# Performance work log

Hardware: AMD Instinct MI355X
Metric: run time of the kernel (lower is better)

## Reference

```python
import jax, jax.numpy as jnp
import numpy as np

B, N, NEV, E, D, L = 4, 20000, 100000, 400000, 64, 3

def setup_inputs() -> dict:
    key = jax.random.key(0)
    ks = jax.random.split(key, 12)
    x = jax.random.normal(ks[0], (B, N, 3), dtype=jnp.float32)
    # channel 0 is the susceptible boolean mask (0/1)
    mask0 = (jax.random.uniform(ks[1], (B, N)) < 0.3).astype(jnp.float32)
    x = x.at[..., 0].set(mask0)
    dag_edge_index = jax.random.randint(ks[2], (2, E), 0, NEV, dtype=jnp.int64)
    event_to_node = jax.random.randint(ks[3], (NEV,), 0, N, dtype=jnp.int64)
    event_src_node = jax.random.randint(ks[4], (NEV,), 0, N, dtype=jnp.int64)
    s = 1.0 / np.sqrt(D)
    Wp = jax.random.normal(ks[5], (6, D), dtype=jnp.float32) * (1.0 / np.sqrt(6))
    bp = jnp.zeros((D,), dtype=jnp.float32)
    Ws = jax.random.normal(ks[6], (L, D, D), dtype=jnp.float32) * s
    Wa = jax.random.normal(ks[7], (L, D, D), dtype=jnp.float32) * s
    ba = jnp.zeros((L, D), dtype=jnp.float32)
    Wo = jax.random.normal(ks[8], (D,), dtype=jnp.float32) * s
    bo = jnp.zeros((), dtype=jnp.float32)
    return {"x": x, "Wp": Wp, "bp": bp, "Ws": Ws, "Wa": Wa, "ba": ba,
            "Wo": Wo, "bo": bo, "dag_edge_index": dag_edge_index,
            "event_to_node": event_to_node, "event_src_node": event_src_node}

def reference(x, Wp, bp, Ws, Wa, ba, Wo, bo, dag_edge_index, event_to_node, event_src_node):
    n_events = event_src_node.shape[0]
    # event features: [B, n_events, 6] -> project -> ReLU
    ev_feat = jnp.concatenate([x[:, event_src_node, :], x[:, event_to_node, :]], axis=-1)
    h = jax.nn.relu(ev_feat @ Wp + bp)  # [B, n_events, D]
    # reversed DAG edges: src = dag[1], dst = dag[0]
    src_e, dst_e = dag_edge_index[1], dag_edge_index[0]
    deg = jnp.zeros((n_events,), h.dtype).at[dst_e].add(1.0)
    deg = jnp.maximum(deg, 1.0)[None, :, None]
    for l in range(Ws.shape[0]):
        agg = jnp.zeros_like(h).at[:, dst_e].add(h[:, src_e])  # scatter-add mean agg
        h = jax.nn.relu(h @ Ws[l] + (agg / deg) @ Wa[l] + ba[l])
    # aggregate events back to nodes (mean)
    node_emb = jnp.zeros((x.shape[0], x.shape[1], h.shape[-1]), h.dtype).at[:, event_to_node].add(h)
    count = jnp.zeros((x.shape[1],), h.dtype).at[event_to_node].add(1.0)
    node_emb = node_emb / jnp.maximum(count, 1.0)[None, :, None]
    scores = node_emb @ Wo + bo  # [B, N]
    susceptible = x[..., 0] > 0
    scores = jnp.where(susceptible, -jnp.inf, scores)
    return jax.nn.log_softmax(scores, axis=-1)
```

## Files before the change

kernel.cpp:

```cpp
#include <hip/hip_runtime.h>
#include <hip/hip_bf16.h>
#include <math.h>

constexpr int B   = 4;
constexpr int N   = 20000;
constexpr int NEV = 100000;
constexpr int E   = 400000;
constexpr int D   = 64;
constexpr int L   = 3;
constexpr int XS  = 136;
constexpr int CAP = 32;
constexpr int CHUNK = 625;

typedef short  short8 __attribute__((ext_vector_type(8)));
typedef float  f32x4  __attribute__((ext_vector_type(4)));
typedef float  f32x2  __attribute__((ext_vector_type(2)));


__device__ inline unsigned short f2bu(float f) {
  union { __hip_bfloat16 b; unsigned short s; } u;
  u.b = __float2bfloat16(f);
  return u.s;
}
__device__ inline unsigned packbf(float lo, float hi) {
  return ((unsigned)f2bu(hi) << 16) | (unsigned)f2bu(lo);
}


__global__ void k_zero(float4* __restrict__ p, int n4) {
  int i = blockIdx.x * blockDim.x + threadIdx.x;
  if (i < n4) p[i] = make_float4(0.f, 0.f, 0.f, 0.f);
}

__global__ void k_fill(const int* __restrict__ dag,
                       int* __restrict__ cnt,
                       int* __restrict__ csrc) {
  int i = blockIdx.x * blockDim.x + threadIdx.x;
  if (i >= E) return;
  int dst = dag[i];
  int src = dag[E + i];
  int pos = atomicAdd(&cnt[dst], 1);
  if (pos < CAP) csrc[dst * CAP + pos] = src;
}

__global__ void k_aux(const int* __restrict__ e2n,
                      int* __restrict__ ncount,
                      const float* __restrict__ Ws,
                      const float* __restrict__ Wa,
                      unsigned short* __restrict__ Wt) {
  int bid = blockIdx.x;
  if (bid < 391) {
    int i = bid * 256 + threadIdx.x;
    if (i < NEV) atomicAdd(&ncount[e2n[i]], 1);
  } else {
    int i = (bid - 391) * 256 + threadIdx.x;
    int l = i >> 13;
    int r = i & 8191;
    int n = r >> 7;
    int s = r & 127;
    int sl = (s < 64) ? s : s - 64;
    int c  = (sl & 3) * 16 + (sl >> 2);
    float v = (s < 64) ? Ws[l * 4096 + c * 64 + n]
                       : Wa[l * 4096 + c * 64 + n];
    Wt[l * 8192 + n * 128 + s] = f2bu(v);
  }
}

__global__ __launch_bounds__(256) void k_proj(const float* __restrict__ x,
                                              const float* __restrict__ Wp,
                                              const float* __restrict__ bp,
                                              const int* __restrict__ esrc,
                                              const int* __restrict__ e2n,
                                              unsigned* __restrict__ h) {
  int gid = blockIdx.x * blockDim.x + threadIdx.x;
  int p   = gid & 15;
  int row = gid >> 4;
  int e   = row >> 2;
  int b   = row & 3;
  int sn = esrc[e], tn = e2n[e];
  const float* xs = x + (size_t)(b * N + sn) * 3;
  const float* xt = x + (size_t)(b * N + tn) * 3;
  float xv[6] = {xs[0], xs[1], xs[2], xt[0], xt[1], xt[2]};
  float a[4];
#pragma unroll
  for (int t = 0; t < 4; ++t) {
    int d = p + 16 * t;
    float acc = bp[d];
#pragma unroll
    for (int k = 0; k < 6; ++k) acc += xv[k] * Wp[k * 64 + d];
    a[t] = fmaxf(acc, 0.f);
  }
  int w = __builtin_amdgcn_cvt_pk_fp8_f32(a[0], a[1], 0, false);
  w     = __builtin_amdgcn_cvt_pk_fp8_f32(a[2], a[3], w, true);
  h[row * 16 + p] = (unsigned)w;
}

template <bool LAST>
__global__ __launch_bounds__(256, 6) void k_layer(
    const unsigned short* __restrict__ Wt,
    const float* __restrict__ ba,
    const float* __restrict__ Wo,
    const int* __restrict__ e2n,
    const int* __restrict__ cnt,
    const int* __restrict__ csrc,
    const unsigned char* __restrict__ h_in,
    unsigned char* __restrict__ h_out,
    float* __restrict__ nscore) {
  __shared__ unsigned short sX[64 * XS];
  const int tid  = threadIdx.x;
  const int wv   = tid >> 6, lane = tid & 63;
  const int e0   = blockIdx.x * 16;
  const int r0   = e0 * 4;

  {
    uint4 v = *(const uint4*)(h_in + (size_t)r0 * 64 + tid * 16);
    int row = tid >> 2, ch = tid & 3;
    unsigned vv[4] = {v.x, v.y, v.z, v.w};
    unsigned out[8];
#pragma unroll
    for (int i = 0; i < 4; ++i) {
      f32x2 lo = __builtin_amdgcn_cvt_pk_f32_fp8((int)vv[i], false);
      f32x2 hi = __builtin_amdgcn_cvt_pk_f32_fp8((int)vv[i], true);
      out[2 * i]     = packbf(lo[0], lo[1]);
      out[2 * i + 1] = packbf(hi[0], hi[1]);
    }
    unsigned short* dst = sX + row * XS + ch * 16;
    *(uint4*)dst       = *(uint4*)&out[0];
    *(uint4*)(dst + 8) = *(uint4*)&out[4];
  }

  const int qg = lane >> 4, sub = lane & 15;
  int vidx = csrc[(size_t)(e0 + wv * 4 + qg) * CAP + sub];
  int c_l  = cnt[e0 + wv * 4 + (lane & 3)];

#pragma unroll
  for (int ei = 0; ei < 4; ++ei) {
    int c = __shfl(c_l, ei, 64);
    int cc16 = min(c, 16);
    float a[16];
#pragma unroll
    for (int i = 0; i < 16; ++i) a[i] = 0.f;
    for (int p = 0; p < cc16; p += 4) {
      int j = p + qg;
      if (j < cc16) {
        int s = __shfl(vidx, ei * 16 + j, 64);
        uint4 v = *(const uint4*)(h_in + (size_t)s * 256 + sub * 16);
        unsigned vv[4] = {v.x, v.y, v.z, v.w};
#pragma unroll
        for (int i = 0; i < 4; ++i) {
          f32x2 lo = __builtin_amdgcn_cvt_pk_f32_fp8((int)vv[i], false);
          f32x2 hi = __builtin_amdgcn_cvt_pk_f32_fp8((int)vv[i], true);
          a[4 * i + 0] += lo[0]; a[4 * i + 1] += lo[1];
          a[4 * i + 2] += hi[0]; a[4 * i + 3] += hi[1];
        }
      }
    }
    int cc = min(c, CAP);
    for (int j = 16 + qg; j < cc; j += 4) {
      int s = csrc[(size_t)(e0 + wv * 4 + ei) * CAP + j];
      uint4 v = *(const uint4*)(h_in + (size_t)s * 256 + sub * 16);
      unsigned vv[4] = {v.x, v.y, v.z, v.w};
#pragma unroll
      for (int i = 0; i < 4; ++i) {
        f32x2 lo = __builtin_amdgcn_cvt_pk_f32_fp8((int)vv[i], false);
        f32x2 hi = __builtin_amdgcn_cvt_pk_f32_fp8((int)vv[i], true);
        a[4 * i + 0] += lo[0]; a[4 * i + 1] += lo[1];
        a[4 * i + 2] += hi[0]; a[4 * i + 3] += hi[1];
      }
    }
#pragma unroll
    for (int i = 0; i < 16; ++i) {
      a[i] += __shfl_xor(a[i], 16, 64);
      a[i] += __shfl_xor(a[i], 32, 64);
    }
    if (qg == 0) {
      float inv = 1.f / fmaxf((float)c, 1.f);
      int lrow = (wv * 4 + ei) * 4 + (sub >> 2);
      unsigned out[8];
#pragma unroll
      for (int i = 0; i < 8; ++i)
        out[i] = packbf(a[2 * i] * inv, a[2 * i + 1] * inv);
      unsigned short* dst = sX + lrow * XS + 64 + (sub & 3) * 16;
      *(uint4*)dst       = *(uint4*)&out[0];
      *(uint4*)(dst + 8) = *(uint4*)&out[4];
    }
  }
  __syncthreads();

  const int m = lane & 15, q = lane >> 4;
  f32x4 acc[4];
#pragma unroll
  for (int t = 0; t < 4; ++t) {
    float bv = ba[t * 16 + m];
    acc[t] = (f32x4){bv, bv, bv, bv};
  }
  const unsigned short* xbase = sX + (wv * 16 + m) * XS + q * 8;
  const unsigned short* wbase = Wt + m * 128 + q * 8;
#pragma unroll
  for (int kk = 0; kk < 4; ++kk) {
    short8 av = *(const short8*)(xbase + kk * 32);
#pragma unroll
    for (int t = 0; t < 4; ++t) {
      short8 bv = *(const short8*)(wbase + t * 2048 + kk * 32);
      acc[t] = __builtin_amdgcn_mfma_f32_16x16x32_bf16(av, bv, acc[t], 0, 0, 0);
    }
  }

  if constexpr (!LAST) {
#pragma unroll
    for (int r = 0; r < 4; ++r) {
      int w = __builtin_amdgcn_cvt_pk_fp8_f32(fmaxf(acc[0][r], 0.f),
                                              fmaxf(acc[1][r], 0.f), 0, false);
      w     = __builtin_amdgcn_cvt_pk_fp8_f32(fmaxf(acc[2][r], 0.f),
                                              fmaxf(acc[3][r], 0.f), w, true);
      int grow = r0 + wv * 16 + q * 4 + r;
      ((unsigned*)h_out)[grow * 16 + m] = (unsigned)w;
    }
  } else {
    float w0 = Wo[m], w1 = Wo[16 + m], w2 = Wo[32 + m], w3 = Wo[48 + m];
#pragma unroll
    for (int r = 0; r < 4; ++r) {
      float v = fmaxf(acc[0][r], 0.f) * w0 + fmaxf(acc[1][r], 0.f) * w1
              + fmaxf(acc[2][r], 0.f) * w2 + fmaxf(acc[3][r], 0.f) * w3;
      v += __shfl_xor(v, 1, 64);
      v += __shfl_xor(v, 2, 64);
      v += __shfl_xor(v, 4, 64);
      v += __shfl_xor(v, 8, 64);
      if (m == 0) {
        int grow = r0 + wv * 16 + q * 4 + r;
        int e = grow >> 2, b = grow & 3;
        atomicAdd(&nscore[b * N + e2n[e]], v);
      }
    }
  }
}

__device__ inline float ls_score(const float* nscore, const int* ncount,
                                 const float* x, float bov, int b, int n) {
  return (x[(size_t)(b * N + n) * 3] > 0.f)
             ? -INFINITY
             : nscore[b * N + n] / fmaxf((float)ncount[n], 1.f) + bov;
}

__global__ __launch_bounds__(256) void k_ls1(const float* __restrict__ nscore,
                                             const int* __restrict__ ncount,
                                             const float* __restrict__ x,
                                             const float* __restrict__ bo,
                                             float* __restrict__ pmax,
                                             float* __restrict__ psum) {
  const int b = blockIdx.x >> 5, ch = blockIdx.x & 31;
  const int n0 = ch * CHUNK;
  const int tid = threadIdx.x;
  const float bov = bo[0];
  float s0 = -INFINITY, s1 = -INFINITY, s2 = -INFINITY;
  if (tid < CHUNK)       s0 = ls_score(nscore, ncount, x, bov, b, n0 + tid);
  if (tid + 256 < CHUNK) s1 = ls_score(nscore, ncount, x, bov, b, n0 + tid + 256);
  if (tid + 512 < CHUNK) s2 = ls_score(nscore, ncount, x, bov, b, n0 + tid + 512);
  float m = fmaxf(fmaxf(s0, s1), s2);
  __shared__ float red[4];
#pragma unroll
  for (int o = 32; o; o >>= 1) m = fmaxf(m, __shfl_xor(m, o, 64));
  if ((tid & 63) == 0) red[tid >> 6] = m;
  __syncthreads();
  float pm = fmaxf(fmaxf(red[0], red[1]), fmaxf(red[2], red[3]));
  float pm2 = (pm == -INFINITY) ? 0.f : pm;
  float e = expf(s0 - pm2) + expf(s1 - pm2) + expf(s2 - pm2);
#pragma unroll
  for (int o = 32; o; o >>= 1) e += __shfl_xor(e, o, 64);
  __syncthreads();
  if ((tid & 63) == 0) red[tid >> 6] = e;
  __syncthreads();
  if (tid == 0) {
    pmax[blockIdx.x] = pm;
    psum[blockIdx.x] = red[0] + red[1] + red[2] + red[3];
  }
}

__global__ __launch_bounds__(256) void k_ls3(const float* __restrict__ pmax,
                                             const float* __restrict__ psum,
                                             const float* __restrict__ nscore,
                                             const int* __restrict__ ncount,
                                             const float* __restrict__ x,
                                             const float* __restrict__ bo,
                                             float* __restrict__ out) {
  const int b = blockIdx.x >> 5, ch = blockIdx.x & 31;
  const int n0 = ch * CHUNK;
  const int tid = threadIdx.x;
  const float bov = bo[0];
  __shared__ float sgm, slse;
  if (tid < 64) {
    float pm = (tid < 32) ? pmax[b * 32 + tid] : -INFINITY;
    float ps = (tid < 32) ? psum[b * 32 + tid] : 0.f;
    float gm = pm;
#pragma unroll
    for (int o = 32; o; o >>= 1) gm = fmaxf(gm, __shfl_xor(gm, o, 64));
    float gm2 = (gm == -INFINITY) ? 0.f : gm;
    float c = (pm == -INFINITY) ? 0.f : ps * expf(pm - gm2);
#pragma unroll
    for (int o = 32; o; o >>= 1) c += __shfl_xor(c, o, 64);
    if (tid == 0) { sgm = gm; slse = logf(c); }
  }
  __syncthreads();
  const float gm = sgm, lse = slse;
  for (int i = tid; i < CHUNK; i += 256) {
    int n = n0 + i;
    float s = ls_score(nscore, ncount, x, bov, b, n);
    out[b * N + n] = fmaxf(s - gm - lse, -3.0e38f);
  }
}

extern "C" void kernel_launch(void* const* d_in, const int* in_sizes, int n_in,
                              void* d_out, int out_size, void* d_ws, size_t ws_size,
                              hipStream_t stream) {
  const float* x   = (const float*)d_in[0];
  const float* Wp  = (const float*)d_in[1];
  const float* bp  = (const float*)d_in[2];
  const float* Ws  = (const float*)d_in[3];
  const float* Wa  = (const float*)d_in[4];
  const float* ba  = (const float*)d_in[5];
  const float* Wo  = (const float*)d_in[6];
  const float* bo  = (const float*)d_in[7];
  const int*   dag = (const int*)d_in[8];
  const int*   e2n = (const int*)d_in[9];
  const int*   esr = (const int*)d_in[10];

  int*   ws     = (int*)d_ws;
  int*   cnt    = ws;
  int*   ncount = ws + 100000;
  float* nscore = (float*)(ws + 120000);
  float* pmax   = (float*)(ws + 200000);
  float* psum   = (float*)(ws + 200128);
  int*   csrc   = ws + 200704;
  unsigned short* Wt = (unsigned short*)(ws + 3400704);
  unsigned char* h0 = (unsigned char*)(ws + 3406912);
  unsigned char* h1 = h0 + (size_t)B * NEV * D;
  float* out    = (float*)d_out;

  k_zero<<<(50000 + 255) / 256, 256, 0, stream>>>((float4*)ws, 50000);
  k_fill<<<(E + 255) / 256, 256, 0, stream>>>(dag, cnt, csrc);
  k_aux<<<391 + 96, 256, 0, stream>>>(e2n, ncount, Ws, Wa, Wt);
  k_proj<<<(B * NEV * 16) / 256, 256, 0, stream>>>(x, Wp, bp, esr, e2n,
                                                   (unsigned*)h0);

  k_layer<false><<<NEV / 16, 256, 0, stream>>>(Wt,         ba,       Wo, e2n,
                                               cnt, csrc, h0, h1, nscore);
  k_layer<false><<<NEV / 16, 256, 0, stream>>>(Wt + 8192,  ba + D,   Wo, e2n,
                                               cnt, csrc, h1, h0, nscore);
  k_layer<true><<<NEV / 16, 256, 0, stream>>>(Wt + 16384,  ba + 2*D, Wo, e2n,
                                              cnt, csrc, h0, h1, nscore);

  k_ls1<<<B * 32, 256, 0, stream>>>(nscore, ncount, x, bo, pmax, psum);
  k_ls3<<<B * 32, 256, 0, stream>>>(pmax, psum, nscore, ncount, x, bo, out);
}
```

Before: 340.7 us.

## Fuse prep kernels, move nscore zeroing into projection, restructure neighbor gather

Merges the CSR fill and auxiliary kernels into one launch and moves zeroing of nscore into the projection kernel, so k_zero clears a smaller region and one launch is removed. In each layer, a row's neighbor gather now has every lane load 4 bytes of all 64 lanes' slice of a neighbor row, four neighbors unrolled, instead of quarter-waves loading 16 bytes each. This removes the cross-quarter shuffle reduction and the 16-float accumulator. Occupancy hint raised from 6 to 8 waves and the index loads hoisted earlier. The risk is more, smaller memory requests per neighbor.

```diff
diff --git a/kernel.cpp b/kernel.cpp
--- a/kernel.cpp
+++ b/kernel.cpp
@@ -32,28 +32,28 @@
   if (i < n4) p[i] = make_float4(0.f, 0.f, 0.f, 0.f);
 }
 
-__global__ void k_fill(const int* __restrict__ dag,
+__global__ void k_prep(const int* __restrict__ dag,
                        int* __restrict__ cnt,
-                       int* __restrict__ csrc) {
-  int i = blockIdx.x * blockDim.x + threadIdx.x;
-  if (i >= E) return;
-  int dst = dag[i];
-  int src = dag[E + i];
-  int pos = atomicAdd(&cnt[dst], 1);
-  if (pos < CAP) csrc[dst * CAP + pos] = src;
-}
-
-__global__ void k_aux(const int* __restrict__ e2n,
-                      int* __restrict__ ncount,
-                      const float* __restrict__ Ws,
-                      const float* __restrict__ Wa,
-                      unsigned short* __restrict__ Wt) {
+                       int* __restrict__ csrc,
+                       const int* __restrict__ e2n,
+                       int* __restrict__ ncount,
+                       const float* __restrict__ Ws,
+                       const float* __restrict__ Wa,
+                       unsigned short* __restrict__ Wt) {
   int bid = blockIdx.x;
-  if (bid < 391) {
+  if (bid < 1563) {
     int i = bid * 256 + threadIdx.x;
+    if (i < E) {
+      int dst = dag[i];
+      int src = dag[E + i];
+      int pos = atomicAdd(&cnt[dst], 1);
+      if (pos < CAP) csrc[dst * CAP + pos] = src;
+    }
+  } else if (bid < 1954) {
+    int i = (bid - 1563) * 256 + threadIdx.x;
     if (i < NEV) atomicAdd(&ncount[e2n[i]], 1);
   } else {
-    int i = (bid - 391) * 256 + threadIdx.x;
+    int i = (bid - 1954) * 256 + threadIdx.x;
     int l = i >> 13;
     int r = i & 8191;
     int n = r >> 7;
@@ -71,8 +71,10 @@
                                               const float* __restrict__ bp,
                                               const int* __restrict__ esrc,
                                               const int* __restrict__ e2n,
-                                              unsigned* __restrict__ h) {
+                                              unsigned* __restrict__ h,
+                                              float* __restrict__ nscore) {
   int gid = blockIdx.x * blockDim.x + threadIdx.x;
+  if (gid < B * N) nscore[gid] = 0.f;
   int p   = gid & 15;
   int row = gid >> 4;
   int e   = row >> 2;
@@ -96,7 +98,7 @@
 }
 
 template <bool LAST>
-__global__ __launch_bounds__(256, 6) void k_layer(
+__global__ __launch_bounds__(256, 8) void k_layer(
     const unsigned short* __restrict__ Wt,
     const float* __restrict__ ba,
     const float* __restrict__ Wo,
@@ -112,6 +114,10 @@
   const int e0   = blockIdx.x * 16;
   const int r0   = e0 * 4;
 
+  const int qg = lane >> 4, sub = lane & 15;
+  int vidx = csrc[(size_t)(e0 + wv * 4 + qg) * CAP + sub];
+  int c_l  = cnt[e0 + wv * 4 + (lane & 3)];
+
   {
     uint4 v = *(const uint4*)(h_in + (size_t)r0 * 64 + tid * 16);
     int row = tid >> 2, ch = tid & 3;
@@ -129,61 +135,55 @@
     *(uint4*)(dst + 8) = *(uint4*)&out[4];
   }
 
-  const int qg = lane >> 4, sub = lane & 15;
-  int vidx = csrc[(size_t)(e0 + wv * 4 + qg) * CAP + sub];
-  int c_l  = cnt[e0 + wv * 4 + (lane & 3)];
-
 #pragma unroll
   for (int ei = 0; ei < 4; ++ei) {
     int c = __shfl(c_l, ei, 64);
     int cc16 = min(c, 16);
-    float a[16];
-#pragma unroll
-    for (int i = 0; i < 16; ++i) a[i] = 0.f;
-    for (int p = 0; p < cc16; p += 4) {
-      int j = p + qg;
-      if (j < cc16) {
-        int s = __shfl(vidx, ei * 16 + j, 64);
-        uint4 v = *(const uint4*)(h_in + (size_t)s * 256 + sub * 16);
-        unsigned vv[4] = {v.x, v.y, v.z, v.w};
-#pragma unroll
-        for (int i = 0; i < 4; ++i) {
-          f32x2 lo = __builtin_amdgcn_cvt_pk_f32_fp8((int)vv[i], false);
-          f32x2 hi = __builtin_amdgcn_cvt_pk_f32_fp8((int)vv[i], true);
-          a[4 * i + 0] += lo[0]; a[4 * i + 1] += lo[1];
-          a[4 * i + 2] += hi[0]; a[4 * i + 3] += hi[1];
-        }
-      }
+    float a0 = 0.f, a1 = 0.f, a2 = 0.f, a3 = 0.f;
+    int j = 0;
+    for (; j + 3 < cc16; j += 4) {
+      int s0 = __shfl(vidx, ei * 16 + j + 0, 64);
+      int s1 = __shfl(vidx, ei * 16 + j + 1, 64);
+      int s2 = __shfl(vidx, ei * 16 + j + 2, 64);
+      int s3 = __shfl(vidx, ei * 16 + j + 3, 64);
+      unsigned v0 = *(const unsigned*)(h_in + (size_t)s0 * 256 + lane * 4);
+      unsigned v1 = *(const unsigned*)(h_in + (size_t)s1 * 256 + lane * 4);
+      unsigned v2 = *(const unsigned*)(h_in + (size_t)s2 * 256 + lane * 4);
+      unsigned v3 = *(const unsigned*)(h_in + (size_t)s3 * 256 + lane * 4);
+      f32x2 l0 = __builtin_amdgcn_cvt_pk_f32_fp8((int)v0, false);
+      f32x2 h0 = __builtin_amdgcn_cvt_pk_f32_fp8((int)v0, true);
+      f32x2 l1 = __builtin_amdgcn_cvt_pk_f32_fp8((int)v1, false);
+      f32x2 h1 = __builtin_amdgcn_cvt_pk_f32_fp8((int)v1, true);
+      f32x2 l2 = __builtin_amdgcn_cvt_pk_f32_fp8((int)v2, false);
+      f32x2 h2 = __builtin_amdgcn_cvt_pk_f32_fp8((int)v2, true);
+      f32x2 l3 = __builtin_amdgcn_cvt_pk_f32_fp8((int)v3, false);
+      f32x2 h3 = __builtin_amdgcn_cvt_pk_f32_fp8((int)v3, true);
+      a0 += l0[0] + l1[0] + l2[0] + l3[0];
+      a1 += l0[1] + l1[1] + l2[1] + l3[1];
+      a2 += h0[0] + h1[0] + h2[0] + h3[0];
+      a3 += h0[1] + h1[1] + h2[1] + h3[1];
+    }
+    for (; j < cc16; ++j) {
+      int s = __shfl(vidx, ei * 16 + j, 64);
+      unsigned v = *(const unsigned*)(h_in + (size_t)s * 256 + lane * 4);
+      f32x2 lo = __builtin_amdgcn_cvt_pk_f32_fp8((int)v, false);
+      f32x2 hi = __builtin_amdgcn_cvt_pk_f32_fp8((int)v, true);
+      a0 += lo[0]; a1 += lo[1]; a2 += hi[0]; a3 += hi[1];
     }
     int cc = min(c, CAP);
-    for (int j = 16 + qg; j < cc; j += 4) {
-      int s = csrc[(size_t)(e0 + wv * 4 + ei) * CAP + j];
-      uint4 v = *(const uint4*)(h_in + (size_t)s * 256 + sub * 16);
-      unsigned vv[4] = {v.x, v.y, v.z, v.w};
-#pragma unroll
-      for (int i = 0; i < 4; ++i) {
-        f32x2 lo = __builtin_amdgcn_cvt_pk_f32_fp8((int)vv[i], false);
-        f32x2 hi = __builtin_amdgcn_cvt_pk_f32_fp8((int)vv[i], true);
-        a[4 * i + 0] += lo[0]; a[4 * i + 1] += lo[1];
-        a[4 * i + 2] += hi[0]; a[4 * i + 3] += hi[1];
-      }
-    }
-#pragma unroll
-    for (int i = 0; i < 16; ++i) {
-      a[i] += __shfl_xor(a[i], 16, 64);
-      a[i] += __shfl_xor(a[i], 32, 64);
-    }
-    if (qg == 0) {
-      float inv = 1.f / fmaxf((float)c, 1.f);
-      int lrow = (wv * 4 + ei) * 4 + (sub >> 2);
-      unsigned out[8];
-#pragma unroll
-      for (int i = 0; i < 8; ++i)
-        out[i] = packbf(a[2 * i] * inv, a[2 * i + 1] * inv);
-      unsigned short* dst = sX + lrow * XS + 64 + (sub & 3) * 16;
-      *(uint4*)dst       = *(uint4*)&out[0];
-      *(uint4*)(dst + 8) = *(uint4*)&out[4];
-    }
+    for (int j2 = 16; j2 < cc; ++j2) {
+      int s = csrc[(size_t)(e0 + wv * 4 + ei) * CAP + j2];
+      unsigned v = *(const unsigned*)(h_in + (size_t)s * 256 + lane * 4);
+      f32x2 lo = __builtin_amdgcn_cvt_pk_f32_fp8((int)v, false);
+      f32x2 hi = __builtin_amdgcn_cvt_pk_f32_fp8((int)v, true);
+      a0 += lo[0]; a1 += lo[1]; a2 += hi[0]; a3 += hi[1];
+    }
+    float inv = 1.f / fmaxf((float)c, 1.f);
+    int lrow = (wv * 4 + ei) * 4 + qg;
+    uint2 w;
+    w.x = packbf(a0 * inv, a1 * inv);
+    w.y = packbf(a2 * inv, a3 * inv);
+    *(uint2*)(sX + lrow * XS + 64 + sub * 4) = w;
   }
   __syncthreads();
 
@@ -336,11 +336,10 @@
   unsigned char* h1 = h0 + (size_t)B * NEV * D;
   float* out    = (float*)d_out;
 
-  k_zero<<<(50000 + 255) / 256, 256, 0, stream>>>((float4*)ws, 50000);
-  k_fill<<<(E + 255) / 256, 256, 0, stream>>>(dag, cnt, csrc);
-  k_aux<<<391 + 96, 256, 0, stream>>>(e2n, ncount, Ws, Wa, Wt);
+  k_zero<<<(30000 + 255) / 256, 256, 0, stream>>>((float4*)ws, 30000);
+  k_prep<<<2050, 256, 0, stream>>>(dag, cnt, csrc, e2n, ncount, Ws, Wa, Wt);
   k_proj<<<(B * NEV * 16) / 256, 256, 0, stream>>>(x, Wp, bp, esr, e2n,
-                                                   (unsigned*)h0);
+                                                   (unsigned*)h0, nscore);
 
   k_layer<false><<<NEV / 16, 256, 0, stream>>>(Wt,         ba,       Wo, e2n,
                                                cnt, csrc, h0, h1, nscore);
```

After: 344.3 us. Within noise of the previous version (+1.1%).
